# Kernel optimization log

Measured on AMD Instinct MI355X. Metric: run time of the kernel, lower is better.

The kernel has to match this reference:

```python
import jax, jax.numpy as jnp
import numpy as np

DEPTH = 10
NUM_TREES = 64
BATCH = 2048
NUM_FORKS = 2 ** DEPTH - 1  # 1023


def setup_inputs() -> dict:
    key = jax.random.key(0)
    x = jax.random.normal(key, (BATCH, NUM_TREES * NUM_FORKS), dtype=jnp.float32)
    return {"x": x}


def reference(x):
    # [B, T, num_forks]
    logits = x.reshape(-1, NUM_TREES, NUM_FORKS)
    sigmoids = jax.nn.sigmoid(logits)
    # trees_flat: probability mass over current frontier of the tree, starts [B, T, 1]
    trees_flat = jnp.ones_like(logits[:, :, :1])
    j = 0
    trees = None
    for i in range(DEPTH):
        d1 = sigmoids[:, :, j:j + 2 ** i]                 # [B, T, 2^i]
        decisions = jnp.stack([1.0 - d1, d1], axis=3)     # [B, T, 2^i, 2]
        trees = trees_flat[:, :, :, None] * decisions     # [B, T, 2^i, 2]
        trees_flat = trees.reshape(trees.shape[0], NUM_TREES, -1)  # [B, T, 2^(i+1)]
        j += 2 ** i
    # sum over penultimate-level nodes, take right-branch probability
    probabilities = trees.sum(axis=2)                     # [B, T, 2]
    return probabilities[:, :, 1]                         # [B, T]
```

## Files before the change

kernel.cpp:

```cpp
#include <hip/hip_runtime.h>

constexpr int DEPTH      = 10;
constexpr int NUM_TREES  = 64;
constexpr int BATCH      = 2048;
constexpr int NUM_FORKS  = (1 << DEPTH) - 1;
constexpr int PAIRS      = BATCH * NUM_TREES;
constexpr int WPB        = 4;
constexpr int REGION     = 1056;

constexpr float LOG2E = 1.44269504088896340736f;

__global__ __launch_bounds__(256, 4) void ndt_kernel(const float* __restrict__ x,
                                                     float* __restrict__ out) {
    __shared__ float lds[WPB * REGION + 8];
    const int tid  = threadIdx.x;
    const int wave = tid >> 6;
    const int lane = tid & 63;
    const int pair = blockIdx.x * WPB + wave;
    const float* __restrict__ xp = x + (size_t)pair * NUM_FORKS;

    float* s = &lds[wave * REGION + 4];

    #pragma unroll
    for (int m = 0; m < 16; ++m) {
        int f = m * 64 + lane;
        if (m < 15 || f < NUM_FORKS) s[1 + f] = xp[f];
    }
    __builtin_amdgcn_wave_barrier();

    float E9[8], D9[8];
    {
        const float4 a = *reinterpret_cast<const float4*>(&s[512 + 8 * lane]);
        const float4 b = *reinterpret_cast<const float4*>(&s[516 + 8 * lane]);
        const float xs[8] = {a.x, a.y, a.z, a.w, b.x, b.y, b.z, b.w};
        #pragma unroll
        for (int c = 0; c < 8; ++c) {
            E9[c] = __builtin_amdgcn_exp2f(-LOG2E * xs[c]);
            D9[c] = 1.0f + E9[c];
        }
    }
    float N8[4], D8[4];
    {
        const float4 a = *reinterpret_cast<const float4*>(&s[256 + 4 * lane]);
        const float xs[4] = {a.x, a.y, a.z, a.w};
        #pragma unroll
        for (int d = 0; d < 4; ++d) {
            float E8 = __builtin_amdgcn_exp2f(-LOG2E * xs[d]);
            N8[d] = fmaf(E8, D9[2 * d + 1], D9[2 * d]);
            D8[d] = D9[2 * d] * D9[2 * d + 1] * (1.0f + E8);
        }
    }
    float v7[2];
    #pragma unroll
    for (int e = 0; e < 2; ++e) {
        float E7 = __builtin_amdgcn_exp2f(-LOG2E * s[128 + 2 * lane + e]);
        float N7 = fmaf(E7 * N8[2 * e], D8[2 * e + 1], N8[2 * e + 1] * D8[2 * e]);
        float D7 = D8[2 * e] * D8[2 * e + 1] * (1.0f + E7);
        v7[e] = N7 * __builtin_amdgcn_rcpf(D7);
    }

    float E6 = __builtin_amdgcn_exp2f(-LOG2E * s[64 + lane]);
    float s6 = __builtin_amdgcn_rcpf(1.0f + E6);
    float v6 = fmaf(s6, v7[1] - v7[0], v7[0]);

    float p = 1.0f;
    #pragma unroll
    for (int i = 0; i < 6; ++i) {
        int a = lane >> (6 - i);
        int b = (lane >> (5 - i)) & 1;
        float u = LOG2E * s[(1 << i) + a];
        float w = __builtin_amdgcn_exp2f(b ? -u : u);
        p *= (1.0f + w);
    }
    float v = v6 * __builtin_amdgcn_rcpf(p);

    #pragma unroll
    for (int off = 32; off > 0; off >>= 1) v += __shfl_xor(v, off, 64);
    if (lane == 0) out[pair] = v;
}

extern "C" void kernel_launch(void* const* d_in, const int* in_sizes, int n_in,
                              void* d_out, int out_size, void* d_ws, size_t ws_size,
                              hipStream_t stream) {
    const float* x = (const float*)d_in[0];
    float* out = (float*)d_out;
    dim3 grid(PAIRS / WPB), block(WPB * 64);
    ndt_kernel<<<grid, block, 0, stream>>>(x, out);
}
```

Baseline: 90.20 us.

## Load block tile with float4 global reads into XOR-swizzled shared memory

Each block now loads its four contiguous pairs (4*1023 floats) as 1023 float4 global loads spread across all 256 threads, replacing per-wave scalar loads. Each float4 lands in LDS at an XOR-swizzled address, and all later reads go through a swizzle helper to avoid bank conflicts on the strided per-lane reads. The aim is fewer, wider global memory instructions. The cost is a block-wide __syncthreads in place of a wave barrier, and reads of consumers that were float4 are now scalar.

```diff
diff --git a/kernel.cpp b/kernel.cpp
--- a/kernel.cpp
+++ b/kernel.cpp
@@ -6,60 +6,70 @@
 constexpr int NUM_FORKS  = (1 << DEPTH) - 1;
 constexpr int PAIRS      = BATCH * NUM_TREES;
 constexpr int WPB        = 4;
-constexpr int REGION     = 1056;
 
 constexpr float LOG2E = 1.44269504088896340736f;
 
+__device__ __forceinline__ float ldsw(const float* sb, int d) {
+    return sb[d ^ ((d >> 3) & 28)];
+}
+
 __global__ __launch_bounds__(256, 4) void ndt_kernel(const float* __restrict__ x,
                                                      float* __restrict__ out) {
-    __shared__ float lds[WPB * REGION + 8];
+    __shared__ __align__(16) float sb[4096];
     const int tid  = threadIdx.x;
     const int wave = tid >> 6;
     const int lane = tid & 63;
     const int pair = blockIdx.x * WPB + wave;
-    const float* __restrict__ xp = x + (size_t)pair * NUM_FORKS;
 
-    float* s = &lds[wave * REGION + 4];
+    const float4* __restrict__ gv =
+        reinterpret_cast<const float4*>(x + (size_t)blockIdx.x * (WPB * NUM_FORKS));
+    #pragma unroll
+    for (int k = 0; k < 4; ++k) {
+        int idx = tid + (k << 8);
+        if (idx < 1023) {
+            float4 v = gv[idx];
+            int d = idx << 2;
+            *reinterpret_cast<float4*>(&sb[d ^ ((d >> 3) & 28)]) = v;
+        }
+    }
+    __syncthreads();
 
-    #pragma unroll
-    for (int m = 0; m < 16; ++m) {
-        int f = m * 64 + lane;
-        if (m < 15 || f < NUM_FORKS) s[1 + f] = xp[f];
-    }
-    __builtin_amdgcn_wave_barrier();
+    const int W = wave * NUM_FORKS;
 
     float E9[8], D9[8];
     {
-        const float4 a = *reinterpret_cast<const float4*>(&s[512 + 8 * lane]);
-        const float4 b = *reinterpret_cast<const float4*>(&s[516 + 8 * lane]);
-        const float xs[8] = {a.x, a.y, a.z, a.w, b.x, b.y, b.z, b.w};
+        const int d0 = W + 511 + (lane << 3);
         #pragma unroll
         for (int c = 0; c < 8; ++c) {
-            E9[c] = __builtin_amdgcn_exp2f(-LOG2E * xs[c]);
+            float xv = ldsw(sb, d0 + c);
+            E9[c] = __builtin_amdgcn_exp2f(-LOG2E * xv);
             D9[c] = 1.0f + E9[c];
         }
     }
     float N8[4], D8[4];
     {
-        const float4 a = *reinterpret_cast<const float4*>(&s[256 + 4 * lane]);
-        const float xs[4] = {a.x, a.y, a.z, a.w};
+        const int d0 = W + 255 + (lane << 2);
         #pragma unroll
-        for (int d = 0; d < 4; ++d) {
-            float E8 = __builtin_amdgcn_exp2f(-LOG2E * xs[d]);
-            N8[d] = fmaf(E8, D9[2 * d + 1], D9[2 * d]);
-            D8[d] = D9[2 * d] * D9[2 * d + 1] * (1.0f + E8);
+        for (int dd = 0; dd < 4; ++dd) {
+            float xv = ldsw(sb, d0 + dd);
+            float E8 = __builtin_amdgcn_exp2f(-LOG2E * xv);
+            N8[dd] = fmaf(E8, D9[2 * dd + 1], D9[2 * dd]);
+            D8[dd] = D9[2 * dd] * D9[2 * dd + 1] * (1.0f + E8);
         }
     }
     float v7[2];
-    #pragma unroll
-    for (int e = 0; e < 2; ++e) {
-        float E7 = __builtin_amdgcn_exp2f(-LOG2E * s[128 + 2 * lane + e]);
-        float N7 = fmaf(E7 * N8[2 * e], D8[2 * e + 1], N8[2 * e + 1] * D8[2 * e]);
-        float D7 = D8[2 * e] * D8[2 * e + 1] * (1.0f + E7);
-        v7[e] = N7 * __builtin_amdgcn_rcpf(D7);
+    {
+        const int d0 = W + 127 + (lane << 1);
+        #pragma unroll
+        for (int e = 0; e < 2; ++e) {
+            float E7 = __builtin_amdgcn_exp2f(-LOG2E * ldsw(sb, d0 + e));
+            float N7 = fmaf(E7 * N8[2 * e], D8[2 * e + 1], N8[2 * e + 1] * D8[2 * e]);
+            float D7 = D8[2 * e] * D8[2 * e + 1] * (1.0f + E7);
+            v7[e] = N7 * __builtin_amdgcn_rcpf(D7);
+        }
     }
 
-    float E6 = __builtin_amdgcn_exp2f(-LOG2E * s[64 + lane]);
+    float E6 = __builtin_amdgcn_exp2f(-LOG2E * ldsw(sb, W + 63 + lane));
     float s6 = __builtin_amdgcn_rcpf(1.0f + E6);
     float v6 = fmaf(s6, v7[1] - v7[0], v7[0]);
 
@@ -68,9 +78,9 @@
     for (int i = 0; i < 6; ++i) {
         int a = lane >> (6 - i);
         int b = (lane >> (5 - i)) & 1;
-        float u = LOG2E * s[(1 << i) + a];
-        float w = __builtin_amdgcn_exp2f(b ? -u : u);
-        p *= (1.0f + w);
+        float u = LOG2E * ldsw(sb, W + (1 << i) - 1 + a);
+        float wv = __builtin_amdgcn_exp2f(b ? -u : u);
+        p *= (1.0f + wv);
     }
     float v = v6 * __builtin_amdgcn_rcpf(p);
 
```

Result: slower. 92.52 us (+2.6%).
